# Performance work log

Hardware: AMD Instinct MI355X
Metric: run time of the kernel (lower is better)

The kernel has to match this reference:

```python
import jax, jax.numpy as jnp
import numpy as np

B, C, H, W = 16, 128, 56, 56
K = 3
F = K * K          # number of deformation filters = kernel taps
OUT = 512
STRIDE = 1


def setup_inputs() -> dict:
    key = jax.random.key(0)
    k1, k2, k3, k4 = jax.random.split(key, 4)
    x = jax.random.normal(k1, (B, C, H, W), jnp.float32)
    # Deform2d 1x1 offset conv: weight [2F, C], bias [2F] initialized to kernel tap offsets
    w_off = jax.random.normal(k2, (2 * F, C), jnp.float32) * 0.01
    half = K // 2
    xs = [float(dx) for dy in range(-half, K - half) for dx in range(-half, K - half)]
    ys = [float(dy) for dy in range(-half, K - half) for dx in range(-half, K - half)]
    b_off = jnp.array(xs + ys, jnp.float32)  # all x offsets first, then all y offsets
    # final 1x1 conv: [OUT, F*C]
    w_conv = jax.random.normal(k3, (OUT, F * C), jnp.float32) * (1.0 / np.sqrt(F * C))
    b_conv = jax.random.normal(k4, (OUT,), jnp.float32) * 0.01
    return {"x": x, "w_off": w_off, "b_off": b_off, "w_conv": w_conv, "b_conv": b_conv}


def _bilinear_sample(img, gx, gy):
    # img: [C,H,W]; gx, gy: [H,W] normalized coords in [-1,1]
    # torch grid_sample defaults: bilinear, zeros padding, align_corners=False
    C_, H_, W_ = img.shape
    ix = ((gx + 1.0) * W_ - 1.0) * 0.5
    iy = ((gy + 1.0) * H_ - 1.0) * 0.5
    x0 = jnp.floor(ix)
    y0 = jnp.floor(iy)
    wx1 = ix - x0
    wx0 = 1.0 - wx1
    wy1 = iy - y0
    wy0 = 1.0 - wy1

    def gather(yy, xx):
        valid = ((xx >= 0) & (xx < W_) & (yy >= 0) & (yy < H_)).astype(img.dtype)
        xi = jnp.clip(xx, 0, W_ - 1).astype(jnp.int32)
        yi = jnp.clip(yy, 0, H_ - 1).astype(jnp.int32)
        return img[:, yi, xi] * valid[None]  # [C,H,W]

    return (gather(y0, x0) * (wy0 * wx0)[None]
            + gather(y0, x0 + 1.0) * (wy0 * wx1)[None]
            + gather(y0 + 1.0, x0) * (wy1 * wx0)[None]
            + gather(y0 + 1.0, x0 + 1.0) * (wy1 * wx1)[None])


def reference(x, w_off, b_off, w_conv, b_conv):
    Bv, Cv, Hv, Wv = x.shape
    scale = 2.0 / max(Hv, Wv)
    # Deform2d: 1x1 conv -> per-pixel offsets, scaled to normalized grid units
    deform = (jnp.einsum('bchw,dc->bdhw', x, w_off) + b_off[None, :, None, None]) * scale
    # matches torch view(B*F, 2, H, W): consecutive channel pairs per filter
    deform = deform.reshape(Bv, F, 2, Hv, Wv)
    # identity grid from affine_grid (align_corners=False)
    base_x = (2.0 * jnp.arange(Wv, dtype=x.dtype) + 1.0) / Wv - 1.0
    base_y = (2.0 * jnp.arange(Hv, dtype=x.dtype) + 1.0) / Hv - 1.0
    # grid is detached in the torch code -> no gradient to the offset conv
    gx = jax.lax.stop_gradient(base_x[None, None, None, :] + deform[:, :, 0])  # [B,F,H,W]
    gy = jax.lax.stop_gradient(base_y[None, None, :, None] + deform[:, :, 1])  # [B,F,H,W]
    sample_f = jax.vmap(_bilinear_sample, in_axes=(None, 0, 0))   # over F filters (input shared)
    sample_bf = jax.vmap(sample_f, in_axes=(0, 0, 0))             # over batch
    sampled = sample_bf(x, gx, gy)                                 # [B,F,C,H,W]
    sampled = sampled.reshape(Bv, F * Cv, Hv, Wv)[:, :, ::STRIDE, ::STRIDE]
    # final 1x1 conv
    return jnp.einsum('bchw,oc->bohw', sampled, w_conv) + b_conv[None, :, None, None]
```

## Files before the change

kernel.cpp:

```cpp
#include <hip/hip_runtime.h>
#include <stdint.h>
#include <stddef.h>

#define BN 16
#define CN 128
#define HN 56
#define WN 56
#define HWN 3136
#define FN 9
#define DN 18
#define ON 512
#define KN 1152
#define MN 50176

typedef __bf16 bf16x8 __attribute__((ext_vector_type(8)));
typedef float f32x4 __attribute__((ext_vector_type(4)));

__device__ __forceinline__ unsigned short f2bf(float f) {
  unsigned int u = __builtin_bit_cast(unsigned int, f);
  u += 0x7fffu + ((u >> 16) & 1u);
  return (unsigned short)(u >> 16);
}

__device__ __forceinline__ void gload_lds16(const void* g, void* l) {
  __builtin_amdgcn_global_load_lds(
      (const __attribute__((address_space(1))) unsigned int*)g,
      (__attribute__((address_space(3))) unsigned int*)l, 16, 0, 0);
}

__global__ void k_transpose(const float* __restrict__ x, unsigned short* __restrict__ xt) {
  __shared__ float tile[32][33];
  const int b = blockIdx.z;
  const int hw0 = blockIdx.x * 32;
  const int c0 = blockIdx.y * 32;
  const int tx = threadIdx.x & 31;
  const int ty = threadIdx.x >> 5;
  const float* xb = x + (size_t)b * CN * HWN;
  unsigned short* xtb = xt + (size_t)b * HWN * CN;
#pragma unroll
  for (int r = 0; r < 4; ++r)
    tile[ty + r * 8][tx] = xb[(size_t)(c0 + ty + r * 8) * HWN + hw0 + tx];
  __syncthreads();
#pragma unroll
  for (int r = 0; r < 4; ++r)
    xtb[(size_t)(hw0 + ty + r * 8) * CN + c0 + tx] = f2bf(tile[tx][ty + r * 8]);
}

__global__ void k_wconv(const float4* __restrict__ w, ushort4* __restrict__ wb) {
  const int i = blockIdx.x * 256 + threadIdx.x;
  float4 v = w[i];
  ushort4 o;
  o.x = f2bf(v.x); o.y = f2bf(v.y); o.z = f2bf(v.z); o.w = f2bf(v.w);
  wb[i] = o;
}

__global__ void k_offsets(const unsigned short* __restrict__ xt, const float* __restrict__ w_off,
                          const float* __restrict__ b_off, float2* __restrict__ ixy) {
  __shared__ float lwoff[DN * CN];
  __shared__ float lboff[DN];
  for (int i = threadIdx.x; i < DN * CN; i += 256) lwoff[i] = w_off[i];
  if (threadIdx.x < DN) lboff[threadIdx.x] = b_off[threadIdx.x];
  __syncthreads();

  const int m = blockIdx.x * 256 + threadIdx.x;
  const int b = m / HWN;
  const int hw = m - b * HWN;
  const int h = hw / WN;
  const int w = hw - h * WN;
  const unsigned short* xp = xt + (size_t)m * CN;
  float acc[DN];
#pragma unroll
  for (int d = 0; d < DN; ++d) acc[d] = lboff[d];
  for (int c = 0; c < CN; c += 8) {
    bf16x8 xv = *(const bf16x8*)(xp + c);
    float xf[8];
#pragma unroll
    for (int q = 0; q < 8; ++q) xf[q] = (float)xv[q];
#pragma unroll
    for (int d = 0; d < DN; ++d) {
      float4 w0 = *(const float4*)(lwoff + d * CN + c);
      float4 w1 = *(const float4*)(lwoff + d * CN + c + 4);
      acc[d] += xf[0] * w0.x + xf[1] * w0.y + xf[2] * w0.z + xf[3] * w0.w
              + xf[4] * w1.x + xf[5] * w1.y + xf[6] * w1.z + xf[7] * w1.w;
    }
  }
  const float scale = 2.0f / 56.0f;
  const float bx = (2.0f * w + 1.0f) / (float)WN - 1.0f;
  const float by = (2.0f * h + 1.0f) / (float)HN - 1.0f;
#pragma unroll
  for (int f = 0; f < FN; ++f) {
    float gx = bx + acc[2 * f] * scale;
    float gy = by + acc[2 * f + 1] * scale;
    float ixv = ((gx + 1.0f) * (float)WN - 1.0f) * 0.5f;
    float iyv = ((gy + 1.0f) * (float)HN - 1.0f) * 0.5f;
    ixy[(size_t)m * FN + f] = make_float2(ixv, iyv);
  }
}

__global__ void k_sample(const unsigned short* __restrict__ xt, const float2* __restrict__ ixy,
                         unsigned short* __restrict__ S) {
  const int g = blockIdx.x * 256 + threadIdx.x;
  const int cc = g & 7;
  const int mf = g >> 3;
  const int m = mf / FN;
  const int f = mf - m * FN;
  const int b = m / HWN;

  const float2 p = ixy[mf];
  const float ix = p.x, iy = p.y;
  const float x0f = floorf(ix), y0f = floorf(iy);
  const float wx1 = ix - x0f, wy1 = iy - y0f;
  const float wx0 = 1.0f - wx1, wy0 = 1.0f - wy1;
  const int x0 = (int)x0f, y0 = (int)y0f;
  const int x1 = x0 + 1, y1 = y0 + 1;
  const bool vx0 = (x0 >= 0) & (x0 < WN), vx1 = (x1 >= 0) & (x1 < WN);
  const bool vy0 = (y0 >= 0) & (y0 < HN), vy1 = (y1 >= 0) & (y1 < HN);
  const float w00 = wy0 * wx0 * ((vy0 & vx0) ? 1.0f : 0.0f);
  const float w01 = wy0 * wx1 * ((vy0 & vx1) ? 1.0f : 0.0f);
  const float w10 = wy1 * wx0 * ((vy1 & vx0) ? 1.0f : 0.0f);
  const float w11 = wy1 * wx1 * ((vy1 & vx1) ? 1.0f : 0.0f);
  const int x0c = min(max(x0, 0), WN - 1), x1c = min(max(x1, 0), WN - 1);
  const int y0c = min(max(y0, 0), HN - 1), y1c = min(max(y1, 0), HN - 1);

  const unsigned short* bp = xt + (size_t)b * HWN * CN + cc * 16;
  const bf16x8* p00 = (const bf16x8*)(bp + (size_t)(y0c * WN + x0c) * CN);
  const bf16x8* p01 = (const bf16x8*)(bp + (size_t)(y0c * WN + x1c) * CN);
  const bf16x8* p10 = (const bf16x8*)(bp + (size_t)(y1c * WN + x0c) * CN);
  const bf16x8* p11 = (const bf16x8*)(bp + (size_t)(y1c * WN + x1c) * CN);
  bf16x8 a0 = p00[0], a1 = p00[1];
  bf16x8 b0 = p01[0], b1 = p01[1];
  bf16x8 c0 = p10[0], c1 = p10[1];
  bf16x8 d0 = p11[0], d1 = p11[1];

  unsigned short ov[16];
#pragma unroll
  for (int q = 0; q < 8; ++q) {
    float lo = w00 * (float)a0[q] + w01 * (float)b0[q] + w10 * (float)c0[q] + w11 * (float)d0[q];
    float hi = w00 * (float)a1[q] + w01 * (float)b1[q] + w10 * (float)c1[q] + w11 * (float)d1[q];
    ov[q] = f2bf(lo);
    ov[q + 8] = f2bf(hi);
  }
  uint4* dst = (uint4*)(S + (size_t)m * KN + f * CN + cc * 16);
  dst[0] = *(const uint4*)(ov);
  dst[1] = *(const uint4*)(ov + 8);
}

__global__ __launch_bounds__(256) void k_gemm(const unsigned short* __restrict__ Wb,
                                              const unsigned short* __restrict__ S,
                                              const float* __restrict__ bias,
                                              float* __restrict__ out) {
  __shared__ __align__(16) char smem[32768];
  unsigned short* lw = (unsigned short*)smem;
  unsigned short* ls = (unsigned short*)(smem + 16384);
  const int tid = threadIdx.x;
  const int wave = tid >> 6;
  const int lane = tid & 63;
  const int quad = lane >> 4;
  const int r16 = lane & 15;
  const int bid = blockIdx.x;
  const int ot = (bid >> 3) & 3;
  const int pt = (bid & 7) + ((bid >> 5) << 3);
  const int o0 = ot * 128;
  const int p0 = pt * 128;
  const int wrow = wave >> 1;
  const int wcol = wave & 1;

  f32x4 acc[4][4];
#pragma unroll
  for (int i = 0; i < 4; ++i)
#pragma unroll
    for (int j = 0; j < 4; ++j) acc[i][j] = (f32x4){0.f, 0.f, 0.f, 0.f};

  const int row0 = tid >> 3;
  const int swc = (((tid & 7) ^ (row0 & 7))) * 8;
  const unsigned short* gw = Wb + (size_t)(o0 + row0) * KN + swc;
  const unsigned short* gs = S + (size_t)(p0 + row0) * KN + swc;
  unsigned short* lwd = lw + wave * 512;
  unsigned short* lsd = ls + wave * 512;

  const int rsw = r16 & 7;
  const int ch0 = (quad ^ rsw) * 8;
  const int ch1 = ((quad ^ rsw) ^ 4) * 8;
  const unsigned short* aw = lw + (wrow * 64 + r16) * 64;
  const unsigned short* bs = ls + (wcol * 64 + r16) * 64;

  for (int kt = 0; kt < KN / 64; ++kt) {
#pragma unroll
    for (int r = 0; r < 4; ++r) {
      gload_lds16(gw + (size_t)r * 32 * KN, lwd + r * 2048);
      gload_lds16(gs + (size_t)r * 32 * KN, lsd + r * 2048);
    }
    gw += 64; gs += 64;
    __syncthreads();
#pragma unroll
    for (int h = 0; h < 2; ++h) {
      const int ch = h ? ch1 : ch0;
      bf16x8 afr[4], bfr[4];
#pragma unroll
      for (int i = 0; i < 4; ++i) afr[i] = *(const bf16x8*)(aw + i * 16 * 64 + ch);
#pragma unroll
      for (int j = 0; j < 4; ++j) bfr[j] = *(const bf16x8*)(bs + j * 16 * 64 + ch);
#pragma unroll
      for (int i = 0; i < 4; ++i)
#pragma unroll
        for (int j = 0; j < 4; ++j)
          acc[i][j] = __builtin_amdgcn_mfma_f32_16x16x32_bf16(afr[i], bfr[j], acc[i][j], 0, 0, 0);
    }
    __syncthreads();
  }

  float* lout = (float*)smem;
  for (int half = 0; half < 2; ++half) {
    __syncthreads();
    if (wrow == half) {
#pragma unroll
      for (int i = 0; i < 4; ++i) {
        const int orow = i * 16 + quad * 4;
#pragma unroll
        for (int j = 0; j < 4; ++j) {
          const int col = wcol * 64 + j * 16 + r16;
          lout[(orow + 0) * 128 + col] = acc[i][j][0];
          lout[(orow + 1) * 128 + col] = acc[i][j][1];
          lout[(orow + 2) * 128 + col] = acc[i][j][2];
          lout[(orow + 3) * 128 + col] = acc[i][j][3];
        }
      }
    }
    __syncthreads();
#pragma unroll
    for (int t = 0; t < 8; ++t) {
      const int idx = t * 256 + tid;
      const int orow = idx >> 5;
      const int c4 = idx & 31;
      float4 v = ((const float4*)lout)[idx];
      const int o = o0 + half * 64 + orow;
      const float bv = bias[o];
      v.x += bv; v.y += bv; v.z += bv; v.w += bv;
      const int p = p0 + c4 * 4;
      const int bidx = p / HWN;
      const int hw = p - bidx * HWN;
      *(float4*)(out + (size_t)bidx * ON * HWN + (size_t)o * HWN + hw) = v;
    }
  }
}

extern "C" void kernel_launch(void* const* d_in, const int* in_sizes, int n_in,
                              void* d_out, int out_size, void* d_ws, size_t ws_size,
                              hipStream_t stream) {
  const float* x = (const float*)d_in[0];
  const float* w_off = (const float*)d_in[1];
  const float* b_off = (const float*)d_in[2];
  const float* w_conv = (const float*)d_in[3];
  const float* b_conv = (const float*)d_in[4];
  float* out = (float*)d_out;

  char* ws = (char*)d_ws;
  unsigned short* xt = (unsigned short*)(ws);
  unsigned short* S = (unsigned short*)(ws + 12845056);
  unsigned short* Wb = (unsigned short*)(ws + 128450560);
  float2* ixy = (float2*)(ws + 129630208);

  k_transpose<<<dim3(98, 4, 16), 256, 0, stream>>>(x, xt);
  k_wconv<<<dim3(576), 256, 0, stream>>>((const float4*)w_conv, (ushort4*)Wb);
  k_offsets<<<dim3(196), 256, 0, stream>>>(xt, w_off, b_off, ixy);
  k_sample<<<dim3(14112), 256, 0, stream>>>(xt, ixy, S);
  k_gemm<<<dim3(1568), 256, 0, stream>>>(Wb, S, b_conv, out);
}
```

Before: 243.7 us.

## Rewrite GEMM as 256x256 tile with double-buffered LDS and phase-interleaved prefetch

```diff
diff --git a/kernel.cpp b/kernel.cpp
--- a/kernel.cpp
+++ b/kernel.cpp
@@ -145,95 +145,158 @@
   dst[1] = *(const uint4*)(ov + 8);
 }
 
-__global__ __launch_bounds__(256) void k_gemm(const unsigned short* __restrict__ Wb,
-                                              const unsigned short* __restrict__ S,
-                                              const float* __restrict__ bias,
-                                              float* __restrict__ out) {
-  __shared__ __align__(16) char smem[32768];
-  unsigned short* lw = (unsigned short*)smem;
-  unsigned short* ls = (unsigned short*)(smem + 16384);
+#define VMCNT4 asm volatile("s_waitcnt vmcnt(4)" ::: "memory")
+#define VMCNT0 asm volatile("s_waitcnt vmcnt(0)" ::: "memory")
+#define SBAR   asm volatile("s_barrier" ::: "memory")
+
+__global__ __launch_bounds__(512, 2) void k_gemm(const unsigned short* __restrict__ Wb,
+                                                 const unsigned short* __restrict__ S,
+                                                 const float* __restrict__ bias,
+                                                 float* __restrict__ out) {
+  __shared__ __align__(128) char smem[131072];
   const int tid = threadIdx.x;
   const int wave = tid >> 6;
   const int lane = tid & 63;
   const int quad = lane >> 4;
   const int r16 = lane & 15;
+  const int wm = wave >> 2;
+  const int wn = wave & 3;
+
   const int bid = blockIdx.x;
-  const int ot = (bid >> 3) & 3;
-  const int pt = (bid & 7) + ((bid >> 5) << 3);
-  const int o0 = ot * 128;
-  const int p0 = pt * 128;
-  const int wrow = wave >> 1;
-  const int wcol = wave & 1;
-
-  f32x4 acc[4][4];
-#pragma unroll
-  for (int i = 0; i < 4; ++i)
-#pragma unroll
-    for (int j = 0; j < 4; ++j) acc[i][j] = (f32x4){0.f, 0.f, 0.f, 0.f};
+  const int wgid = (bid & 7) * 49 + (bid >> 3);
+  const int o0 = (wgid & 1) * 256;
+  const int p0 = (wgid >> 1) * 256;
+
+  f32x4 acc[2][2][4][2];
+#pragma unroll
+  for (int a = 0; a < 2; ++a)
+#pragma unroll
+    for (int b = 0; b < 2; ++b)
+#pragma unroll
+      for (int c = 0; c < 4; ++c)
+#pragma unroll
+        for (int d = 0; d < 2; ++d) acc[a][b][c][d] = (f32x4){0.f, 0.f, 0.f, 0.f};
 
   const int row0 = tid >> 3;
-  const int swc = (((tid & 7) ^ (row0 & 7))) * 8;
-  const unsigned short* gw = Wb + (size_t)(o0 + row0) * KN + swc;
-  const unsigned short* gs = S + (size_t)(p0 + row0) * KN + swc;
-  unsigned short* lwd = lw + wave * 512;
-  unsigned short* lsd = ls + wave * 512;
+  const int chunk0 = (tid & 7) ^ (row0 & 7);
+  const unsigned short* gA0 = Wb + (size_t)(o0 + row0) * KN + chunk0 * 8;
+  const unsigned short* gB0 = S + (size_t)(p0 + row0) * KN + chunk0 * 8;
+
+#define STAGE_A(PAR, HALF, KT) do {                                              \
+    const unsigned short* g_ = gA0 + (size_t)(HALF) * 128 * KN + (size_t)(KT) * 64; \
+    char* d_ = smem + (PAR) * 32768 + (HALF) * 16384 + tid * 16;                 \
+    gload_lds16(g_, d_);                                                         \
+    gload_lds16(g_ + (size_t)64 * KN, d_ + 8192);                                \
+  } while (0)
+#define STAGE_B(PAR, HALF, KT) do {                                              \
+    const unsigned short* g_ = gB0 + (size_t)(HALF) * 128 * KN + (size_t)(KT) * 64; \
+    char* d_ = smem + 65536 + (PAR) * 32768 + (HALF) * 16384 + tid * 16;         \
+    gload_lds16(g_, d_);                                                         \
+    gload_lds16(g_ + (size_t)64 * KN, d_ + 8192);                                \
+  } while (0)
 
   const int rsw = r16 & 7;
-  const int ch0 = (quad ^ rsw) * 8;
-  const int ch1 = ((quad ^ rsw) ^ 4) * 8;
-  const unsigned short* aw = lw + (wrow * 64 + r16) * 64;
-  const unsigned short* bs = ls + (wcol * 64 + r16) * 64;
-
-  for (int kt = 0; kt < KN / 64; ++kt) {
-#pragma unroll
-    for (int r = 0; r < 4; ++r) {
-      gload_lds16(gw + (size_t)r * 32 * KN, lwd + r * 2048);
-      gload_lds16(gs + (size_t)r * 32 * KN, lsd + r * 2048);
-    }
-    gw += 64; gs += 64;
+  const int ch0 = (quad ^ rsw) * 16;
+  const int ch1 = ch0 ^ 64;
+  const int a_row = (wm * 64 + r16) * 128;
+  const int b_row = (wn * 32 + r16) * 128;
+
+#define PHASE(PAR, QI, QJ, STAGE_STMT, WAIT_STMT) do {                           \
+    const char* pa_ = smem + (PAR) * 32768 + (QI) * 16384 + a_row;               \
+    const char* pb_ = smem + 65536 + (PAR) * 32768 + (QJ) * 16384 + b_row;       \
+    bf16x8 a0_ = *(const bf16x8*)(pa_ + 0 * 2048 + ch0);                         \
+    bf16x8 a1_ = *(const bf16x8*)(pa_ + 1 * 2048 + ch0);                         \
+    bf16x8 a2_ = *(const bf16x8*)(pa_ + 2 * 2048 + ch0);                         \
+    bf16x8 a3_ = *(const bf16x8*)(pa_ + 3 * 2048 + ch0);                         \
+    bf16x8 b0_ = *(const bf16x8*)(pb_ + 0 * 2048 + ch0);                         \
+    bf16x8 b1_ = *(const bf16x8*)(pb_ + 1 * 2048 + ch0);                         \
+    bf16x8 a4_ = *(const bf16x8*)(pa_ + 0 * 2048 + ch1);                         \
+    bf16x8 a5_ = *(const bf16x8*)(pa_ + 1 * 2048 + ch1);                         \
+    bf16x8 a6_ = *(const bf16x8*)(pa_ + 2 * 2048 + ch1);                         \
+    bf16x8 a7_ = *(const bf16x8*)(pa_ + 3 * 2048 + ch1);                         \
+    bf16x8 b2_ = *(const bf16x8*)(pb_ + 0 * 2048 + ch1);                         \
+    bf16x8 b3_ = *(const bf16x8*)(pb_ + 1 * 2048 + ch1);                         \
+    STAGE_STMT;                                                                  \
+    WAIT_STMT;                                                                   \
+    SBAR;                                                                        \
+    __builtin_amdgcn_s_setprio(1);                                               \
+    acc[QI][QJ][0][0] = __builtin_amdgcn_mfma_f32_16x16x32_bf16(a0_, b0_, acc[QI][QJ][0][0], 0, 0, 0); \
+    acc[QI][QJ][0][1] = __builtin_amdgcn_mfma_f32_16x16x32_bf16(a0_, b1_, acc[QI][QJ][0][1], 0, 0, 0); \
+    acc[QI][QJ][1][0] = __builtin_amdgcn_mfma_f32_16x16x32_bf16(a1_, b0_, acc[QI][QJ][1][0], 0, 0, 0); \
+    acc[QI][QJ][1][1] = __builtin_amdgcn_mfma_f32_16x16x32_bf16(a1_, b1_, acc[QI][QJ][1][1], 0, 0, 0); \
+    acc[QI][QJ][2][0] = __builtin_amdgcn_mfma_f32_16x16x32_bf16(a2_, b0_, acc[QI][QJ][2][0], 0, 0, 0); \
+    acc[QI][QJ][2][1] = __builtin_amdgcn_mfma_f32_16x16x32_bf16(a2_, b1_, acc[QI][QJ][2][1], 0, 0, 0); \
+    acc[QI][QJ][3][0] = __builtin_amdgcn_mfma_f32_16x16x32_bf16(a3_, b0_, acc[QI][QJ][3][0], 0, 0, 0); \
+    acc[QI][QJ][3][1] = __builtin_amdgcn_mfma_f32_16x16x32_bf16(a3_, b1_, acc[QI][QJ][3][1], 0, 0, 0); \
+    acc[QI][QJ][0][0] = __builtin_amdgcn_mfma_f32_16x16x32_bf16(a4_, b2_, acc[QI][QJ][0][0], 0, 0, 0); \
+    acc[QI][QJ][0][1] = __builtin_amdgcn_mfma_f32_16x16x32_bf16(a4_, b3_, acc[QI][QJ][0][1], 0, 0, 0); \
+    acc[QI][QJ][1][0] = __builtin_amdgcn_mfma_f32_16x16x32_bf16(a5_, b2_, acc[QI][QJ][1][0], 0, 0, 0); \
+    acc[QI][QJ][1][1] = __builtin_amdgcn_mfma_f32_16x16x32_bf16(a5_, b3_, acc[QI][QJ][1][1], 0, 0, 0); \
+    acc[QI][QJ][2][0] = __builtin_amdgcn_mfma_f32_16x16x32_bf16(a6_, b2_, acc[QI][QJ][2][0], 0, 0, 0); \
+    acc[QI][QJ][2][1] = __builtin_amdgcn_mfma_f32_16x16x32_bf16(a6_, b3_, acc[QI][QJ][2][1], 0, 0, 0); \
+    acc[QI][QJ][3][0] = __builtin_amdgcn_mfma_f32_16x16x32_bf16(a7_, b2_, acc[QI][QJ][3][0], 0, 0, 0); \
+    acc[QI][QJ][3][1] = __builtin_amdgcn_mfma_f32_16x16x32_bf16(a7_, b3_, acc[QI][QJ][3][1], 0, 0, 0); \
+    __builtin_amdgcn_s_setprio(0);                                               \
+    SBAR;                                                                        \
+  } while (0)
+
+  STAGE_A(0, 0, 0); STAGE_B(0, 0, 0); STAGE_A(0, 1, 0); STAGE_B(0, 1, 0);
+  STAGE_A(1, 0, 1); STAGE_B(1, 0, 1);
+  VMCNT4;
+  SBAR;
+
+#pragma unroll 1
+  for (int it = 0; it < 8; ++it) {
+    const int t1 = 2 * it + 1, t2 = 2 * it + 2, t3 = 2 * it + 3;
+    PHASE(0, 0, 0, STAGE_A(1, 1, t1), (void)0);
+    PHASE(0, 0, 1, STAGE_B(1, 1, t1), (void)0);
+    PHASE(0, 1, 0, STAGE_A(0, 0, t2), (void)0);
+    PHASE(0, 1, 1, STAGE_B(0, 0, t2), VMCNT4);
+    PHASE(1, 0, 0, STAGE_A(0, 1, t2), (void)0);
+    PHASE(1, 0, 1, STAGE_B(0, 1, t2), (void)0);
+    PHASE(1, 1, 0, STAGE_A(1, 0, t3), (void)0);
+    PHASE(1, 1, 1, STAGE_B(1, 0, t3), VMCNT4);
+  }
+  PHASE(0, 0, 0, STAGE_A(1, 1, 17), (void)0);
+  PHASE(0, 0, 1, STAGE_B(1, 1, 17), (void)0);
+  PHASE(0, 1, 0, (void)0, (void)0);
+  PHASE(0, 1, 1, (void)0, VMCNT0);
+  PHASE(1, 0, 0, (void)0, (void)0);
+  PHASE(1, 0, 1, (void)0, (void)0);
+  PHASE(1, 1, 0, (void)0, (void)0);
+  PHASE(1, 1, 1, (void)0, (void)0);
+
+  float* lout = (float*)smem;
+  const int LSTR = 260;
+#pragma unroll
+  for (int ob = 0; ob < 8; ++ob) {
+    const int Qi = ob >> 2, wsel = (ob >> 1) & 1, s2 = ob & 1;
     __syncthreads();
-#pragma unroll
-    for (int h = 0; h < 2; ++h) {
-      const int ch = h ? ch1 : ch0;
-      bf16x8 afr[4], bfr[4];
-#pragma unroll
-      for (int i = 0; i < 4; ++i) afr[i] = *(const bf16x8*)(aw + i * 16 * 64 + ch);
-#pragma unroll
-      for (int j = 0; j < 4; ++j) bfr[j] = *(const bf16x8*)(bs + j * 16 * 64 + ch);
-#pragma unroll
-      for (int i = 0; i < 4; ++i)
-#pragma unroll
-        for (int j = 0; j < 4; ++j)
-          acc[i][j] = __builtin_amdgcn_mfma_f32_16x16x32_bf16(afr[i], bfr[j], acc[i][j], 0, 0, 0);
-    }
-    __syncthreads();
-  }
-
-  float* lout = (float*)smem;
-  for (int half = 0; half < 2; ++half) {
-    __syncthreads();
-    if (wrow == half) {
-#pragma unroll
-      for (int i = 0; i < 4; ++i) {
-        const int orow = i * 16 + quad * 4;
-#pragma unroll
-        for (int j = 0; j < 4; ++j) {
-          const int col = wcol * 64 + j * 16 + r16;
-          lout[(orow + 0) * 128 + col] = acc[i][j][0];
-          lout[(orow + 1) * 128 + col] = acc[i][j][1];
-          lout[(orow + 2) * 128 + col] = acc[i][j][2];
-          lout[(orow + 3) * 128 + col] = acc[i][j][3];
-        }
+    if (wm == wsel) {
+#pragma unroll
+      for (int il = 0; il < 2; ++il) {
+        const int i = s2 * 2 + il;
+#pragma unroll
+        for (int Qj = 0; Qj < 2; ++Qj)
+#pragma unroll
+          for (int j = 0; j < 2; ++j) {
+            f32x4 v = acc[Qi][Qj][i][j];
+            const int col = Qj * 128 + wn * 32 + j * 16 + r16;
+            const int rb = il * 16 + quad * 4;
+            lout[(rb + 0) * LSTR + col] = v[0];
+            lout[(rb + 1) * LSTR + col] = v[1];
+            lout[(rb + 2) * LSTR + col] = v[2];
+            lout[(rb + 3) * LSTR + col] = v[3];
+          }
       }
     }
     __syncthreads();
 #pragma unroll
-    for (int t = 0; t < 8; ++t) {
-      const int idx = t * 256 + tid;
-      const int orow = idx >> 5;
-      const int c4 = idx & 31;
-      float4 v = ((const float4*)lout)[idx];
-      const int o = o0 + half * 64 + orow;
+    for (int tl = 0; tl < 4; ++tl) {
+      const int idx = tl * 512 + tid;
+      const int rr = idx >> 6, c4 = idx & 63;
+      float4 v = *(const float4*)(lout + rr * LSTR + c4 * 4);
+      const int o = o0 + ob * 32 + rr;
       const float bv = bias[o];
       v.x += bv; v.y += bv; v.z += bv; v.w += bv;
       const int p = p0 + c4 * 4;
@@ -242,6 +305,9 @@
       *(float4*)(out + (size_t)bidx * ON * HWN + (size_t)o * HWN + hw) = v;
     }
   }
+#undef PHASE
+#undef STAGE_A
+#undef STAGE_B
 }
 
 extern "C" void kernel_launch(void* const* d_in, const int* in_sizes, int n_in,
@@ -264,5 +330,5 @@
   k_wconv<<<dim3(576), 256, 0, stream>>>((const float4*)w_conv, (ushort4*)Wb);
   k_offsets<<<dim3(196), 256, 0, stream>>>(xt, w_off, b_off, ixy);
   k_sample<<<dim3(14112), 256, 0, stream>>>(xt, ixy, S);
-  k_gemm<<<dim3(1568), 256, 0, stream>>>(Wb, S, b_conv, out);
-}
+  k_gemm<<<dim3(392), 512, 0, stream>>>(Wb, S, b_conv, out);
+}
```

Result: slower. 251.2 us (+3.1%).

## Fuse bilinear sampling into the GEMM, building B tiles in LDS on the fly

Applied to the files above, without the earlier changes.

```diff
diff --git a/kernel.cpp b/kernel.cpp
--- a/kernel.cpp
+++ b/kernel.cpp
@@ -12,6 +12,7 @@
 #define ON 512
 #define KN 1152
 #define MN 50176
+#define MB 128
 
 typedef __bf16 bf16x8 __attribute__((ext_vector_type(8)));
 typedef float f32x4 __attribute__((ext_vector_type(4)));
@@ -20,12 +21,6 @@
   unsigned int u = __builtin_bit_cast(unsigned int, f);
   u += 0x7fffu + ((u >> 16) & 1u);
   return (unsigned short)(u >> 16);
-}
-
-__device__ __forceinline__ void gload_lds16(const void* g, void* l) {
-  __builtin_amdgcn_global_load_lds(
-      (const __attribute__((address_space(1))) unsigned int*)g,
-      (__attribute__((address_space(3))) unsigned int*)l, 16, 0, 0);
 }
 
 __global__ void k_transpose(const float* __restrict__ x, unsigned short* __restrict__ xt) {
@@ -97,151 +92,158 @@
   }
 }
 
-__global__ void k_sample(const unsigned short* __restrict__ xt, const float2* __restrict__ ixy,
-                         unsigned short* __restrict__ S) {
-  const int g = blockIdx.x * 256 + threadIdx.x;
-  const int cc = g & 7;
-  const int mf = g >> 3;
-  const int m = mf / FN;
-  const int f = mf - m * FN;
-  const int b = m / HWN;
-
-  const float2 p = ixy[mf];
-  const float ix = p.x, iy = p.y;
-  const float x0f = floorf(ix), y0f = floorf(iy);
-  const float wx1 = ix - x0f, wy1 = iy - y0f;
-  const float wx0 = 1.0f - wx1, wy0 = 1.0f - wy1;
-  const int x0 = (int)x0f, y0 = (int)y0f;
-  const int x1 = x0 + 1, y1 = y0 + 1;
-  const bool vx0 = (x0 >= 0) & (x0 < WN), vx1 = (x1 >= 0) & (x1 < WN);
-  const bool vy0 = (y0 >= 0) & (y0 < HN), vy1 = (y1 >= 0) & (y1 < HN);
-  const float w00 = wy0 * wx0 * ((vy0 & vx0) ? 1.0f : 0.0f);
-  const float w01 = wy0 * wx1 * ((vy0 & vx1) ? 1.0f : 0.0f);
-  const float w10 = wy1 * wx0 * ((vy1 & vx0) ? 1.0f : 0.0f);
-  const float w11 = wy1 * wx1 * ((vy1 & vx1) ? 1.0f : 0.0f);
-  const int x0c = min(max(x0, 0), WN - 1), x1c = min(max(x1, 0), WN - 1);
-  const int y0c = min(max(y0, 0), HN - 1), y1c = min(max(y1, 0), HN - 1);
-
-  const unsigned short* bp = xt + (size_t)b * HWN * CN + cc * 16;
-  const bf16x8* p00 = (const bf16x8*)(bp + (size_t)(y0c * WN + x0c) * CN);
-  const bf16x8* p01 = (const bf16x8*)(bp + (size_t)(y0c * WN + x1c) * CN);
-  const bf16x8* p10 = (const bf16x8*)(bp + (size_t)(y1c * WN + x0c) * CN);
-  const bf16x8* p11 = (const bf16x8*)(bp + (size_t)(y1c * WN + x1c) * CN);
-  bf16x8 a0 = p00[0], a1 = p00[1];
-  bf16x8 b0 = p01[0], b1 = p01[1];
-  bf16x8 c0 = p10[0], c1 = p10[1];
-  bf16x8 d0 = p11[0], d1 = p11[1];
-
-  unsigned short ov[16];
-#pragma unroll
-  for (int q = 0; q < 8; ++q) {
-    float lo = w00 * (float)a0[q] + w01 * (float)b0[q] + w10 * (float)c0[q] + w11 * (float)d0[q];
-    float hi = w00 * (float)a1[q] + w01 * (float)b1[q] + w10 * (float)c1[q] + w11 * (float)d1[q];
-    ov[q] = f2bf(lo);
-    ov[q + 8] = f2bf(hi);
-  }
-  uint4* dst = (uint4*)(S + (size_t)m * KN + f * CN + cc * 16);
-  dst[0] = *(const uint4*)(ov);
-  dst[1] = *(const uint4*)(ov + 8);
-}
-
-__global__ __launch_bounds__(256) void k_gemm(const unsigned short* __restrict__ Wb,
-                                              const unsigned short* __restrict__ S,
-                                              const float* __restrict__ bias,
-                                              float* __restrict__ out) {
-  __shared__ __align__(16) char smem[32768];
-  unsigned short* lw = (unsigned short*)smem;
-  unsigned short* ls = (unsigned short*)(smem + 16384);
+__global__ __launch_bounds__(512, 2) void k_fused(const unsigned short* __restrict__ Wb,
+                                                  const unsigned short* __restrict__ xt,
+                                                  const float2* __restrict__ ixy,
+                                                  const float* __restrict__ bias,
+                                                  float* __restrict__ out) {
+  __shared__ __align__(16) char smem[41984];
+  float2* lixy = (float2*)(smem + 32768);
   const int tid = threadIdx.x;
   const int wave = tid >> 6;
   const int lane = tid & 63;
   const int quad = lane >> 4;
   const int r16 = lane & 15;
+  const int wm = wave >> 1;
+  const int wn = wave & 1;
+
   const int bid = blockIdx.x;
-  const int ot = (bid >> 3) & 3;
-  const int pt = (bid & 7) + ((bid >> 5) << 3);
-  const int o0 = ot * 128;
-  const int p0 = pt * 128;
-  const int wrow = wave >> 1;
-  const int wcol = wave & 1;
-
-  f32x4 acc[4][4];
-#pragma unroll
-  for (int i = 0; i < 4; ++i)
+  const int wgid = (bid & 7) * 49 + (bid >> 3);
+  const int m0 = wgid * MB;
+
+  for (int i = tid; i < MB * FN; i += 512) lixy[i] = ixy[(size_t)m0 * FN + i];
+
+  const int bm = tid >> 2;
+  const int bc = (tid & 3) * 16;
+  const int gm = m0 + bm;
+  const int bb = gm / HWN;
+  const unsigned short* xb = xt + (size_t)bb * HWN * CN;
+
+  f32x4 acc[8][4];
+#pragma unroll
+  for (int i = 0; i < 8; ++i)
 #pragma unroll
     for (int j = 0; j < 4; ++j) acc[i][j] = (f32x4){0.f, 0.f, 0.f, 0.f};
 
-  const int row0 = tid >> 3;
-  const int swc = (((tid & 7) ^ (row0 & 7))) * 8;
-  const unsigned short* gw = Wb + (size_t)(o0 + row0) * KN + swc;
-  const unsigned short* gs = S + (size_t)(p0 + row0) * KN + swc;
-  unsigned short* lwd = lw + wave * 512;
-  unsigned short* lsd = ls + wave * 512;
-
-  const int rsw = r16 & 7;
-  const int ch0 = (quad ^ rsw) * 8;
-  const int ch1 = ((quad ^ rsw) ^ 4) * 8;
-  const unsigned short* aw = lw + (wrow * 64 + r16) * 64;
-  const unsigned short* bs = ls + (wcol * 64 + r16) * 64;
-
-  for (int kt = 0; kt < KN / 64; ++kt) {
-#pragma unroll
-    for (int r = 0; r < 4; ++r) {
-      gload_lds16(gw + (size_t)r * 32 * KN, lwd + r * 2048);
-      gload_lds16(gs + (size_t)r * 32 * KN, lsd + r * 2048);
-    }
-    gw += 64; gs += 64;
+  const int rsw = r16 & 15 & 7;
+  const int b_row = (wn * 64 + r16) * 128;
+  const unsigned short* aP = Wb + (size_t)(wm * 128 + r16) * KN + quad * 8;
+
+#define BUILD(DST, KT) do {                                                        \
+    const int f_ = (KT) >> 1, h_ = (KT) & 1;                                       \
+    const float2 p_ = lixy[bm * FN + f_];                                          \
+    const float ix_ = p_.x, iy_ = p_.y;                                            \
+    const float x0f = floorf(ix_), y0f = floorf(iy_);                              \
+    const float wx1 = ix_ - x0f, wy1 = iy_ - y0f;                                  \
+    const float wx0 = 1.0f - wx1, wy0 = 1.0f - wy1;                                \
+    const int x0 = (int)x0f, y0 = (int)y0f;                                        \
+    const int x1 = x0 + 1, y1 = y0 + 1;                                            \
+    const bool vx0 = (x0 >= 0) & (x0 < WN), vx1 = (x1 >= 0) & (x1 < WN);           \
+    const bool vy0 = (y0 >= 0) & (y0 < HN), vy1 = (y1 >= 0) & (y1 < HN);           \
+    const float w00 = wy0 * wx0 * ((vy0 & vx0) ? 1.0f : 0.0f);                     \
+    const float w01 = wy0 * wx1 * ((vy0 & vx1) ? 1.0f : 0.0f);                     \
+    const float w10 = wy1 * wx0 * ((vy1 & vx0) ? 1.0f : 0.0f);                     \
+    const float w11 = wy1 * wx1 * ((vy1 & vx1) ? 1.0f : 0.0f);                     \
+    const int x0c = min(max(x0, 0), WN - 1), x1c = min(max(x1, 0), WN - 1);        \
+    const int y0c = min(max(y0, 0), HN - 1), y1c = min(max(y1, 0), HN - 1);        \
+    const unsigned short* cp_ = xb + h_ * 64 + bc;                                 \
+    const bf16x8* q00 = (const bf16x8*)(cp_ + (size_t)(y0c * WN + x0c) * CN);      \
+    const bf16x8* q01 = (const bf16x8*)(cp_ + (size_t)(y0c * WN + x1c) * CN);      \
+    const bf16x8* q10 = (const bf16x8*)(cp_ + (size_t)(y1c * WN + x0c) * CN);      \
+    const bf16x8* q11 = (const bf16x8*)(cp_ + (size_t)(y1c * WN + x1c) * CN);      \
+    bf16x8 A0 = q00[0], A1 = q00[1];                                               \
+    bf16x8 B0 = q01[0], B1 = q01[1];                                               \
+    bf16x8 C0 = q10[0], C1 = q10[1];                                               \
+    bf16x8 D0 = q11[0], D1 = q11[1];                                               \
+    unsigned short ov[16];                                                         \
+    _Pragma("unroll") for (int q_ = 0; q_ < 8; ++q_) {                             \
+      float lo = w00 * (float)A0[q_] + w01 * (float)B0[q_]                         \
+               + w10 * (float)C0[q_] + w11 * (float)D0[q_];                        \
+      float hi = w00 * (float)A1[q_] + w01 * (float)B1[q_]                         \
+               + w10 * (float)C1[q_] + w11 * (float)D1[q_];                        \
+      ov[q_] = f2bf(lo);                                                           \
+      ov[q_ + 8] = f2bf(hi);                                                       \
+    }                                                                              \
+    const int c0_ = (tid & 3) * 2;                                                 \
+    *(uint4*)(smem + (DST) + bm * 128 + ((c0_ ^ (bm & 7)) * 16)) =                 \
+        *(const uint4*)(ov);                                                       \
+    *(uint4*)(smem + (DST) + bm * 128 + (((c0_ + 1) ^ (bm & 7)) * 16)) =           \
+        *(const uint4*)(ov + 8);                                                   \
+  } while (0)
+
+#define LOADA(AV, KT, H) do {                                                      \
+    _Pragma("unroll") for (int i_ = 0; i_ < 8; ++i_)                               \
+      AV[i_] = *(const bf16x8*)(aP + (size_t)i_ * 16 * KN + (KT) * 64 + (H) * 32); \
+  } while (0)
+
+#define AB_MFMA(PARB, H, AV) do {                                                  \
+    const char* bb_ = smem + (PARB) + b_row;                                       \
+    bf16x8 bv[4];                                                                  \
+    _Pragma("unroll") for (int j_ = 0; j_ < 4; ++j_)                               \
+      bv[j_] = *(const bf16x8*)(bb_ + j_ * 16 * 128 + ((((H) * 4 + quad) ^ rsw) * 16)); \
+    __builtin_amdgcn_s_setprio(1);                                                 \
+    _Pragma("unroll") for (int i_ = 0; i_ < 8; ++i_)                               \
+    _Pragma("unroll") for (int j_ = 0; j_ < 4; ++j_)                               \
+      acc[i_][j_] = __builtin_amdgcn_mfma_f32_16x16x32_bf16(AV[i_], bv[j_],        \
+                                                            acc[i_][j_], 0, 0, 0); \
+    __builtin_amdgcn_s_setprio(0);                                                 \
+  } while (0)
+
+  __syncthreads();
+  BUILD(0, 0);
+  __syncthreads();
+
+#pragma unroll 1
+  for (int kt = 0; kt < 18; ++kt) {
+    const int PAR = (kt & 1) * 16384;
+    bf16x8 a0v[8], a1v[8];
+    LOADA(a0v, kt, 0);
+    if (kt < 17) BUILD(16384 - PAR, kt + 1);
+    LOADA(a1v, kt, 1);
+    AB_MFMA(PAR, 0, a0v);
+    AB_MFMA(PAR, 1, a1v);
     __syncthreads();
-#pragma unroll
-    for (int h = 0; h < 2; ++h) {
-      const int ch = h ? ch1 : ch0;
-      bf16x8 afr[4], bfr[4];
-#pragma unroll
-      for (int i = 0; i < 4; ++i) afr[i] = *(const bf16x8*)(aw + i * 16 * 64 + ch);
-#pragma unroll
-      for (int j = 0; j < 4; ++j) bfr[j] = *(const bf16x8*)(bs + j * 16 * 64 + ch);
-#pragma unroll
-      for (int i = 0; i < 4; ++i)
-#pragma unroll
-        for (int j = 0; j < 4; ++j)
-          acc[i][j] = __builtin_amdgcn_mfma_f32_16x16x32_bf16(afr[i], bfr[j], acc[i][j], 0, 0, 0);
-    }
+  }
+
+  float* lout = (float*)smem;
+  const int LSTR = 132;
+#pragma unroll 1
+  for (int ob = 0; ob < 16; ++ob) {
     __syncthreads();
-  }
-
-  float* lout = (float*)smem;
-  for (int half = 0; half < 2; ++half) {
-    __syncthreads();
-    if (wrow == half) {
-#pragma unroll
-      for (int i = 0; i < 4; ++i) {
-        const int orow = i * 16 + quad * 4;
+    if (wm == (ob >> 2)) {
+#pragma unroll
+      for (int il = 0; il < 2; ++il) {
+        const int i = (ob & 3) * 2 + il;
 #pragma unroll
         for (int j = 0; j < 4; ++j) {
-          const int col = wcol * 64 + j * 16 + r16;
-          lout[(orow + 0) * 128 + col] = acc[i][j][0];
-          lout[(orow + 1) * 128 + col] = acc[i][j][1];
-          lout[(orow + 2) * 128 + col] = acc[i][j][2];
-          lout[(orow + 3) * 128 + col] = acc[i][j][3];
+          f32x4 v = acc[i][j];
+          const int col = wn * 64 + j * 16 + r16;
+          const int rb = il * 16 + quad * 4;
+          lout[(rb + 0) * LSTR + col] = v[0];
+          lout[(rb + 1) * LSTR + col] = v[1];
+          lout[(rb + 2) * LSTR + col] = v[2];
+          lout[(rb + 3) * LSTR + col] = v[3];
         }
       }
     }
     __syncthreads();
 #pragma unroll
-    for (int t = 0; t < 8; ++t) {
-      const int idx = t * 256 + tid;
-      const int orow = idx >> 5;
-      const int c4 = idx & 31;
-      float4 v = ((const float4*)lout)[idx];
-      const int o = o0 + half * 64 + orow;
+    for (int tl = 0; tl < 2; ++tl) {
+      const int idx = tl * 512 + tid;
+      const int orow = idx >> 5, c4 = idx & 31;
+      float4 v = *(const float4*)(lout + orow * LSTR + c4 * 4);
+      const int o = ob * 32 + orow;
       const float bv = bias[o];
       v.x += bv; v.y += bv; v.z += bv; v.w += bv;
-      const int p = p0 + c4 * 4;
+      const int p = m0 + c4 * 4;
       const int bidx = p / HWN;
       const int hw = p - bidx * HWN;
       *(float4*)(out + (size_t)bidx * ON * HWN + (size_t)o * HWN + hw) = v;
     }
   }
+#undef BUILD
+#undef LOADA
+#undef AB_MFMA
 }
 
 extern "C" void kernel_launch(void* const* d_in, const int* in_sizes, int n_in,
@@ -256,13 +258,11 @@
 
   char* ws = (char*)d_ws;
   unsigned short* xt = (unsigned short*)(ws);
-  unsigned short* S = (unsigned short*)(ws + 12845056);
-  unsigned short* Wb = (unsigned short*)(ws + 128450560);
-  float2* ixy = (float2*)(ws + 129630208);
+  unsigned short* Wb = (unsigned short*)(ws + 12845056);
+  float2* ixy = (float2*)(ws + 14024704);
 
   k_transpose<<<dim3(98, 4, 16), 256, 0, stream>>>(x, xt);
   k_wconv<<<dim3(576), 256, 0, stream>>>((const float4*)w_conv, (ushort4*)Wb);
   k_offsets<<<dim3(196), 256, 0, stream>>>(xt, w_off, b_off, ixy);
-  k_sample<<<dim3(14112), 256, 0, stream>>>(xt, ixy, S);
-  k_gemm<<<dim3(1568), 256, 0, stream>>>(Wb, S, b_conv, out);
-}
+  k_fused<<<dim3(392), 512, 0, stream>>>(Wb, xt, ixy, b_conv, out);
+}
```

After: 582.4 us. 139% more time.
